# Kernel optimization log

Measured on AMD Instinct MI355X. Metric: run time of the kernel, lower is better.

Reference implementation:

```python
import jax, jax.numpy as jnp
import numpy as np

B, S, D, H, C = 2, 2048, 1024, 16, 64

def setup_inputs() -> dict:
    key = jax.random.key(0)
    kx, kq, kk, kv, ko = jax.random.split(key, 5)
    scale = 0.02
    return {
        "x": jax.random.normal(kx, (B, S, D), dtype=jnp.float32),
        "Wq": jax.random.normal(kq, (D, H, C), dtype=jnp.float32) * scale,
        "Wk": jax.random.normal(kk, (D, H, C), dtype=jnp.float32) * scale,
        "Wv": jax.random.normal(kv, (D, H, C), dtype=jnp.float32) * scale,
        "Wo": jax.random.normal(ko, (H, C, D), dtype=jnp.float32) * scale,
    }

def reference(x, Wq, Wk, Wv, Wo):
    # project to per-head q/k/v: [B,S,H,C]
    q = jnp.einsum('bqd,dhc->bqhc', x, Wq)
    k = jnp.einsum('bkd,dhc->bkhc', x, Wk)
    v = jnp.einsum('bkd,dhc->bkhc', x, Wv)
    q = q * (C ** -0.5)
    alphas = jnp.einsum('bqhc,bkhc->bhqk', q, k)  # [B,H,S,S]
    weights = jax.nn.softmax(alphas, axis=-1)
    out = jnp.einsum('bhqk,bkhc->bqhc', weights, v)
    return jnp.einsum('bqhc,hcd->bqd', out, Wo)
```

## Files before the change

kernel.cpp:

```cpp
#include <hip/hip_runtime.h>
#include <hip/hip_bf16.h>
#include <stdint.h>
#include <stddef.h>

typedef __bf16 bf16;
typedef __bf16 bf16x4 __attribute__((ext_vector_type(4)));
typedef __bf16 bf16x8 __attribute__((ext_vector_type(8)));
typedef float f32x4 __attribute__((ext_vector_type(4)));

#define DEV __device__ __forceinline__

DEV void async16(const bf16* g, bf16* l) {
    __builtin_amdgcn_global_load_lds(
        (const __attribute__((address_space(1))) void*)g,
        (__attribute__((address_space(3))) void*)l,
        16, 0, 0);
}

DEV uint32_t pktrunc(float lo, float hi) {
    return __builtin_amdgcn_perm(__builtin_bit_cast(uint32_t, hi),
                                 __builtin_bit_cast(uint32_t, lo), 0x07060302u);
}


__global__ void prep(const float* __restrict__ x,
                     const float* __restrict__ Wq, const float* __restrict__ Wk,
                     const float* __restrict__ Wv, const float* __restrict__ Wo,
                     bf16* __restrict__ xb, bf16* __restrict__ WqkvT,
                     bf16* __restrict__ WoT) {
    __shared__ float t[32][33];
    if (blockIdx.z == 4) {
        const int bid = blockIdx.y * 32 + blockIdx.x;
#pragma unroll
        for (int i = 0; i < 4; ++i) {
            const int idx = ((bid * 4 + i) * 256 + threadIdx.x) * 4;
            const float4 v = *(const float4*)(x + idx);
            bf16 o4[4] = {(bf16)v.x, (bf16)v.y, (bf16)v.z, (bf16)v.w};
            *(uint2*)(xb + idx) = *(const uint2*)o4;
        }
        return;
    }
    const float* src;
    bf16* dst;
    float scale = 1.0f;
    switch (blockIdx.z) {
        case 0: src = Wq; dst = WqkvT; scale = 0.125f * 1.4426950408889634f; break;
        case 1: src = Wk; dst = WqkvT + 1024 * 1024; break;
        case 2: src = Wv; dst = WqkvT + 2 * 1024 * 1024; break;
        default: src = Wo; dst = WoT; break;
    }
    const int c0 = blockIdx.x * 32, r0 = blockIdx.y * 32;
    const int tx = threadIdx.x & 31, ty = threadIdx.x >> 5;
#pragma unroll
    for (int i = 0; i < 32; i += 8)
        t[ty + i][tx] = src[(size_t)(r0 + ty + i) * 1024 + c0 + tx];
    __syncthreads();
#pragma unroll
    for (int i = 0; i < 32; i += 8)
        dst[(size_t)(c0 + ty + i) * 1024 + r0 + tx] = (bf16)(t[tx][ty + i] * scale);
}


template <bool OUT_F32>
__global__ __launch_bounds__(256, 3) void gemm_bt(
    const bf16* __restrict__ A, const bf16* __restrict__ BT, void* __restrict__ Cout,
    int M, int N, int K, bf16* __restrict__ VTout) {
    __shared__ __attribute__((aligned(16))) bf16 As[2 * 128 * 32];
    __shared__ __attribute__((aligned(16))) bf16 Bs[2 * 128 * 32];
    const int tid = threadIdx.x;
    const int wid = tid >> 6;
    const int lane = tid & 63;
    const int quad = lane >> 4;
    const int l16 = lane & 15;
    const int wm = wid >> 1, wn = wid & 1;

    const int orig = blockIdx.x;
    const int xcd = orig & 7, pos = orig >> 3;
    const int row = (xcd >> 1) * 8 + (pos & 7);
    const int col = (xcd & 1) * 12 + (pos >> 3);
    const int m0 = row * 128, n0 = col * 128;

    const int srow = wid * 32 + (lane >> 2);
    const int skcol = (lane & 3) * 8;
    const bf16* ag = A + (size_t)(m0 + srow) * K + skcol;
    const bf16* bg = BT + (size_t)(n0 + srow) * K + skcol;

    f32x4 acc[4][4];
#pragma unroll
    for (int i = 0; i < 4; ++i)
#pragma unroll
        for (int j = 0; j < 4; ++j) acc[i][j] = (f32x4){0.f, 0.f, 0.f, 0.f};

    for (int k0 = 0; k0 < K; k0 += 64) {
#pragma unroll
        for (int p = 0; p < 2; ++p) {
            async16(ag + k0 + p * 32, &As[p * 4096 + (wid * 32) * 32]);
            async16(ag + (size_t)16 * K + k0 + p * 32, &As[p * 4096 + (wid * 32 + 16) * 32]);
            async16(bg + k0 + p * 32, &Bs[p * 4096 + (wid * 32) * 32]);
            async16(bg + (size_t)16 * K + k0 + p * 32, &Bs[p * 4096 + (wid * 32 + 16) * 32]);
        }
        __syncthreads();

#pragma unroll
        for (int ks = 0; ks < 2; ++ks) {
            bf16x8 af[4], bfr[4];
#pragma unroll
            for (int mi = 0; mi < 4; ++mi)
                af[mi] = *(const bf16x8*)&As[ks * 4096 + (wm * 64 + mi * 16 + l16) * 32 + quad * 8];
#pragma unroll
            for (int ni = 0; ni < 4; ++ni)
                bfr[ni] = *(const bf16x8*)&Bs[ks * 4096 + (wn * 64 + ni * 16 + l16) * 32 + quad * 8];
#pragma unroll
            for (int mi = 0; mi < 4; ++mi)
#pragma unroll
                for (int ni = 0; ni < 4; ++ni)
                    acc[mi][ni] = __builtin_amdgcn_mfma_f32_16x16x32_bf16(
                        af[mi], bfr[ni], acc[mi][ni], 0, 0, 0);
        }
        __syncthreads();
    }

    if (VTout && n0 >= 2048) {
#pragma unroll
        for (int mi = 0; mi < 4; ++mi)
#pragma unroll
            for (int ni = 0; ni < 4; ++ni) {
                bf16 pk[4] = {(bf16)acc[mi][ni][0], (bf16)acc[mi][ni][1],
                              (bf16)acc[mi][ni][2], (bf16)acc[mi][ni][3]};
                *(uint2*)&VTout[(size_t)(n0 - 2048 + wn * 64 + ni * 16 + l16) * 4096 +
                                (m0 + wm * 64 + mi * 16 + quad * 4)] = *(const uint2*)pk;
            }
        return;
    }
    if (OUT_F32) {
        float* C = (float*)Cout;
#pragma unroll
        for (int mi = 0; mi < 4; ++mi)
#pragma unroll
            for (int ni = 0; ni < 4; ++ni)
#pragma unroll
                for (int r = 0; r < 4; ++r)
                    C[(size_t)(m0 + wm * 64 + mi * 16 + quad * 4 + r) * N +
                      (n0 + wn * 64 + ni * 16 + l16)] = acc[mi][ni][r];
    } else {
        bf16* C = (bf16*)Cout;
#pragma unroll
        for (int mi = 0; mi < 4; ++mi)
#pragma unroll
            for (int ni = 0; ni < 4; ++ni)
#pragma unroll
                for (int r = 0; r < 4; ++r)
                    C[(size_t)(m0 + wm * 64 + mi * 16 + quad * 4 + r) * N +
                      (n0 + wn * 64 + ni * 16 + l16)] = (bf16)acc[mi][ni][r];
    }
}


__global__ __launch_bounds__(256, 4) void gemm_tm2(
    const bf16* __restrict__ A, const bf16* __restrict__ BT, float* __restrict__ C,
    int M, int N, int K) {
    __shared__ __attribute__((aligned(16))) bf16 As[2 * 64 * 32];
    __shared__ __attribute__((aligned(16))) bf16 Bs[2 * 128 * 32];
    const int tid = threadIdx.x;
    const int wid = tid >> 6;
    const int lane = tid & 63;
    const int quad = lane >> 4;
    const int l16 = lane & 15;
    const int wm = wid >> 1, wn = wid & 1;

    const int orig = blockIdx.x;
    const int xcd = orig & 7, pos = orig >> 3;
    const int row = (xcd >> 1) * 16 + (pos & 15);
    const int col = (xcd & 1) * 4 + (pos >> 4);
    const int m0 = row * 64, n0 = col * 128;

    const int srowA = wid * 16 + (lane >> 2);
    const int srowB = wid * 32 + (lane >> 2);
    const int skcol = (lane & 3) * 8;
    const bf16* ag = A + (size_t)(m0 + srowA) * K + skcol;
    const bf16* bg = BT + (size_t)(n0 + srowB) * K + skcol;

    f32x4 acc[2][4];
#pragma unroll
    for (int i = 0; i < 2; ++i)
#pragma unroll
        for (int j = 0; j < 4; ++j) acc[i][j] = (f32x4){0.f, 0.f, 0.f, 0.f};

    for (int k0 = 0; k0 < K; k0 += 64) {
#pragma unroll
        for (int p = 0; p < 2; ++p) {
            async16(ag + k0 + p * 32, &As[p * 2048 + (wid * 16) * 32]);
            async16(bg + k0 + p * 32, &Bs[p * 4096 + (wid * 32) * 32]);
            async16(bg + (size_t)16 * K + k0 + p * 32, &Bs[p * 4096 + (wid * 32 + 16) * 32]);
        }
        __syncthreads();

#pragma unroll
        for (int ks = 0; ks < 2; ++ks) {
            bf16x8 af[2], bfr[4];
#pragma unroll
            for (int mi = 0; mi < 2; ++mi)
                af[mi] = *(const bf16x8*)&As[ks * 2048 + (wm * 32 + mi * 16 + l16) * 32 + quad * 8];
#pragma unroll
            for (int ni = 0; ni < 4; ++ni)
                bfr[ni] = *(const bf16x8*)&Bs[ks * 4096 + (wn * 64 + ni * 16 + l16) * 32 + quad * 8];
#pragma unroll
            for (int mi = 0; mi < 2; ++mi)
#pragma unroll
                for (int ni = 0; ni < 4; ++ni)
                    acc[mi][ni] = __builtin_amdgcn_mfma_f32_16x16x32_bf16(
                        af[mi], bfr[ni], acc[mi][ni], 0, 0, 0);
        }
        __syncthreads();
    }

#pragma unroll
    for (int mi = 0; mi < 2; ++mi)
#pragma unroll
        for (int ni = 0; ni < 4; ++ni)
#pragma unroll
            for (int r = 0; r < 4; ++r)
                C[(size_t)(m0 + wm * 32 + mi * 16 + quad * 4 + r) * N +
                  (n0 + wn * 64 + ni * 16 + l16)] = acc[mi][ni][r];
}


__global__ __launch_bounds__(256, 2) void flash_attn(
    const bf16* __restrict__ QKV, const bf16* __restrict__ VT, bf16* __restrict__ att) {
    constexpr int LDK = 72;
    constexpr int LDV = 136;
    __shared__ __attribute__((aligned(16))) char smem[36864];
    bf16* Ks = (bf16*)smem;
    bf16* Vs = (bf16*)(smem + 18432);
    float* Osc = (float*)smem;
    float* Lred = (float*)(smem + 32768);

    const int tid = threadIdx.x, wid = tid >> 6, lane = tid & 63;
    const int quad = lane >> 4, l16 = lane & 15;
    const int qh = wid >> 1, kh = wid & 1;
    const int bh = blockIdx.x, qt = blockIdx.y;
    const int b = bh >> 4, h = bh & 15;
    const int q0 = qt * 128;

    bf16x8 qf[4][2];
    {
        const bf16* qbase = QKV + (size_t)(b * 2048 + q0 + qh * 64 + l16) * 3072 + h * 64 + quad * 8;
#pragma unroll
        for (int mi = 0; mi < 4; ++mi)
#pragma unroll
            for (int ks = 0; ks < 2; ++ks)
                qf[mi][ks] = *(const bf16x8*)(qbase + (size_t)mi * 16 * 3072 + ks * 32);
    }

    const int krow = tid >> 3, kcol = (tid & 7) * 8;
    const int vrow = tid >> 4, vcol = (tid & 15) * 8;
    const bf16* kg = QKV + (size_t)(b * 2048 + krow) * 3072 + 1024 + h * 64 + kcol;
    const bf16* vg = VT + (size_t)(h * 64 + vrow) * 4096 + b * 2048 + vcol;

    bf16x8 kr[4], vr[4];
#pragma unroll
    for (int p = 0; p < 4; ++p) {
        kr[p] = *(const bf16x8*)(kg + (size_t)(32 * p) * 3072);
        vr[p] = *(const bf16x8*)(vg + (size_t)(16 * p) * 4096);
    }

    const bf16 one = (bf16)1.0f;
    const bf16x8 onesf = (bf16x8){one, one, one, one, one, one, one, one};

    f32x4 o[4][4];
    f32x4 ls[4];
#pragma unroll
    for (int mi = 0; mi < 4; ++mi) {
        ls[mi] = (f32x4){0.f, 0.f, 0.f, 0.f};
#pragma unroll
        for (int ct = 0; ct < 4; ++ct) o[mi][ct] = (f32x4){0.f, 0.f, 0.f, 0.f};
    }

    for (int it = 0; it < 16; ++it) {
#pragma unroll
        for (int p = 0; p < 4; ++p) {
            *(bf16x8*)&Ks[(32 * p + krow) * LDK + kcol] = kr[p];
            *(bf16x8*)&Vs[(16 * p + vrow) * LDV + vcol] = vr[p];
        }
        __syncthreads();

        if (it < 15) {
            const size_t ko = (size_t)(it + 1) * 128;
#pragma unroll
            for (int p = 0; p < 4; ++p) {
                kr[p] = *(const bf16x8*)(kg + (ko + 32 * p) * 3072);
                vr[p] = *(const bf16x8*)(vg + (size_t)(16 * p) * 4096 + ko);
            }
        }

#pragma unroll
        for (int pr = 0; pr < 2; ++pr) {
            const int kb = kh * 64 + pr * 32;
            const bf16x8 kfA0 = *(const bf16x8*)&Ks[(kb + l16) * LDK + quad * 8];
            const bf16x8 kfA1 = *(const bf16x8*)&Ks[(kb + l16) * LDK + 32 + quad * 8];
            const bf16x8 kfB0 = *(const bf16x8*)&Ks[(kb + 16 + l16) * LDK + quad * 8];
            const bf16x8 kfB1 = *(const bf16x8*)&Ks[(kb + 16 + l16) * LDK + 32 + quad * 8];
            bf16x8 vf[4];
#pragma unroll
            for (int ct = 0; ct < 4; ++ct) {
                const bf16x4 lo = *(const bf16x4*)&Vs[(ct * 16 + l16) * LDV + kb + quad * 4];
                const bf16x4 hi = *(const bf16x4*)&Vs[(ct * 16 + l16) * LDV + kb + 16 + quad * 4];
                vf[ct] = (bf16x8){lo[0], lo[1], lo[2], lo[3], hi[0], hi[1], hi[2], hi[3]};
            }
            __builtin_amdgcn_s_setprio(1);
#pragma unroll
            for (int mi = 0; mi < 4; ++mi) {
                f32x4 sA = (f32x4){0.f, 0.f, 0.f, 0.f};
                f32x4 sB = (f32x4){0.f, 0.f, 0.f, 0.f};
                sA = __builtin_amdgcn_mfma_f32_16x16x32_bf16(kfA0, qf[mi][0], sA, 0, 0, 0);
                sA = __builtin_amdgcn_mfma_f32_16x16x32_bf16(kfA1, qf[mi][1], sA, 0, 0, 0);
                sB = __builtin_amdgcn_mfma_f32_16x16x32_bf16(kfB0, qf[mi][0], sB, 0, 0, 0);
                sB = __builtin_amdgcn_mfma_f32_16x16x32_bf16(kfB1, qf[mi][1], sB, 0, 0, 0);

                const float pa0 = __builtin_amdgcn_exp2f(sA[0]);
                const float pa1 = __builtin_amdgcn_exp2f(sA[1]);
                const float pa2 = __builtin_amdgcn_exp2f(sA[2]);
                const float pa3 = __builtin_amdgcn_exp2f(sA[3]);
                const float pb0 = __builtin_amdgcn_exp2f(sB[0]);
                const float pb1 = __builtin_amdgcn_exp2f(sB[1]);
                const float pb2 = __builtin_amdgcn_exp2f(sB[2]);
                const float pb3 = __builtin_amdgcn_exp2f(sB[3]);

                union { uint32_t u[4]; bf16x8 v; } pu;
                pu.u[0] = pktrunc(pa0, pa1);
                pu.u[1] = pktrunc(pa2, pa3);
                pu.u[2] = pktrunc(pb0, pb1);
                pu.u[3] = pktrunc(pb2, pb3);
                const bf16x8 pf = pu.v;
#pragma unroll
                for (int ct = 0; ct < 4; ++ct)
                    o[mi][ct] = __builtin_amdgcn_mfma_f32_16x16x32_bf16(pf, vf[ct], o[mi][ct], 0, 0, 0);
                ls[mi] = __builtin_amdgcn_mfma_f32_16x16x32_bf16(pf, onesf, ls[mi], 0, 0, 0);
            }
            __builtin_amdgcn_s_setprio(0);
        }
        __syncthreads();
    }

    if (l16 == 0) {
#pragma unroll
        for (int mi = 0; mi < 4; ++mi)
#pragma unroll
            for (int r = 0; r < 4; ++r)
                Lred[wid * 64 + mi * 16 + quad * 4 + r] = ls[mi][r];
    }
    if (kh == 1) {
        float* dst = Osc + qh * 4096;
#pragma unroll
        for (int mi = 0; mi < 4; ++mi)
#pragma unroll
            for (int ct = 0; ct < 4; ++ct)
                *(f32x4*)(dst + (mi * 4 + ct) * 256 + lane * 4) = o[mi][ct];
    }
    __syncthreads();

    if (kh == 0) {
        const float* src = Osc + qh * 4096;
#pragma unroll
        for (int mi = 0; mi < 4; ++mi)
#pragma unroll
            for (int ct = 0; ct < 4; ++ct)
                o[mi][ct] += *(const f32x4*)(src + (mi * 4 + ct) * 256 + lane * 4);
#pragma unroll
        for (int mi = 0; mi < 4; ++mi)
#pragma unroll
            for (int r = 0; r < 4; ++r) {
                const int qrow = mi * 16 + quad * 4 + r;
                const float l = Lred[(qh * 2) * 64 + qrow] + Lred[(qh * 2 + 1) * 64 + qrow];
                const float inv = 1.0f / l;
                bf16* orow = att + (size_t)(b * 2048 + q0 + qh * 64 + qrow) * 1024 + h * 64 + l16;
#pragma unroll
                for (int ct = 0; ct < 4; ++ct)
                    orow[ct * 16] = (bf16)(o[mi][ct][r] * inv);
            }
    }
}


extern "C" void kernel_launch(void* const* d_in, const int* in_sizes, int n_in,
                              void* d_out, int out_size, void* d_ws, size_t ws_size,
                              hipStream_t stream) {
    (void)in_sizes; (void)n_in; (void)out_size; (void)ws_size;
    const float* x  = (const float*)d_in[0];
    const float* Wq = (const float*)d_in[1];
    const float* Wk = (const float*)d_in[2];
    const float* Wv = (const float*)d_in[3];
    const float* Wo = (const float*)d_in[4];

    char* ws = (char*)d_ws;
    bf16* xb    = (bf16*)(ws);
    bf16* att   = xb;
    bf16* WqkvT = (bf16*)(ws + (size_t)8  * 1024 * 1024);
    bf16* WoT   = (bf16*)(ws + (size_t)14 * 1024 * 1024);
    bf16* QKV   = (bf16*)(ws + (size_t)16 * 1024 * 1024);
    bf16* VT    = (bf16*)(ws + (size_t)40 * 1024 * 1024);

    prep<<<dim3(32, 32, 5), 256, 0, stream>>>(x, Wq, Wk, Wv, Wo, xb, WqkvT, WoT);

    gemm_bt<false><<<768, 256, 0, stream>>>(
        xb, WqkvT, QKV, 4096, 3072, 1024, VT);

    flash_attn<<<dim3(32, 16), 256, 0, stream>>>(QKV, VT, att);

    gemm_tm2<<<512, 256, 0, stream>>>(
        att, WoT, (float*)d_out, 4096, 1024, 1024);
}
```

Baseline: 175.6 us.

## Replace QKV projection GEMM with 256x256-tile, 8-wave, 4-stage pipelined kernel

The QKV projection GEMM moves from 128x128 tiles with 4 waves and a simple load-then-compute loop to 256x256 tiles with 8 waves per block. It uses a 4-buffer LDS ring (128 KB) that prefetches two k-steps ahead, with XOR-swizzled LDS addressing to avoid bank conflicts. Loads and MFMA groups are interleaved with barriers and s_setprio. The aim is to raise data reuse per tile and hide global-load latency, at the cost of only 192 blocks (fewer than the CU count) and heavy LDS and register use per block.

```diff
diff --git a/kernel.cpp b/kernel.cpp
--- a/kernel.cpp
+++ b/kernel.cpp
@@ -61,98 +61,115 @@
 }
 
 
-template <bool OUT_F32>
-__global__ __launch_bounds__(256, 3) void gemm_bt(
-    const bf16* __restrict__ A, const bf16* __restrict__ BT, void* __restrict__ Cout,
-    int M, int N, int K, bf16* __restrict__ VTout) {
-    __shared__ __attribute__((aligned(16))) bf16 As[2 * 128 * 32];
-    __shared__ __attribute__((aligned(16))) bf16 Bs[2 * 128 * 32];
+__global__ __launch_bounds__(512, 2) void gemm_bt8(
+    const bf16* __restrict__ A, const bf16* __restrict__ BT, bf16* __restrict__ C,
+    bf16* __restrict__ VTout) {
+    __shared__ __attribute__((aligned(16))) char smem[131072];
     const int tid = threadIdx.x;
-    const int wid = tid >> 6;
-    const int lane = tid & 63;
-    const int quad = lane >> 4;
-    const int l16 = lane & 15;
-    const int wm = wid >> 1, wn = wid & 1;
-
-    const int orig = blockIdx.x;
-    const int xcd = orig & 7, pos = orig >> 3;
-    const int row = (xcd >> 1) * 8 + (pos & 7);
-    const int col = (xcd & 1) * 12 + (pos >> 3);
-    const int m0 = row * 128, n0 = col * 128;
-
-    const int srow = wid * 32 + (lane >> 2);
-    const int skcol = (lane & 3) * 8;
-    const bf16* ag = A + (size_t)(m0 + srow) * K + skcol;
-    const bf16* bg = BT + (size_t)(n0 + srow) * K + skcol;
-
-    f32x4 acc[4][4];
-#pragma unroll
-    for (int i = 0; i < 4; ++i)
+    const int wid = tid >> 6, lane = tid & 63;
+    const int quad = lane >> 4, l16 = lane & 15;
+    const int wm = wid >> 2, wn = wid & 3;
+    const int m0 = (blockIdx.x & 15) * 256;
+    const int n0 = (blockIdx.x >> 4) * 256;
+
+    const int srow = tid >> 2;
+    const int chsw = (tid & 3) ^ ((srow >> 1) & 3);
+    const bf16* agA1 = A + (size_t)(m0 + srow) * 1024 + chsw * 8;
+    const bf16* agA2 = A + (size_t)(m0 + 128 + srow) * 1024 + chsw * 8;
+    const bf16* bgB1 = BT + (size_t)(n0 + srow) * 1024 + chsw * 8;
+    const bf16* bgB2 = BT + (size_t)(n0 + 128 + srow) * 1024 + chsw * 8;
+
+    const int chq = quad ^ ((l16 >> 1) & 3);
+    const int rbA = (wm * 128 + l16) * 32 + chq * 8;
+    const int rbB = (wn * 64 + l16) * 32 + chq * 8;
+
+    f32x4 acc[8][4];
+#pragma unroll
+    for (int i = 0; i < 8; ++i)
 #pragma unroll
         for (int j = 0; j < 4; ++j) acc[i][j] = (f32x4){0.f, 0.f, 0.f, 0.f};
 
-    for (int k0 = 0; k0 < K; k0 += 64) {
-#pragma unroll
-        for (int p = 0; p < 2; ++p) {
-            async16(ag + k0 + p * 32, &As[p * 4096 + (wid * 32) * 32]);
-            async16(ag + (size_t)16 * K + k0 + p * 32, &As[p * 4096 + (wid * 32 + 16) * 32]);
-            async16(bg + k0 + p * 32, &Bs[p * 4096 + (wid * 32) * 32]);
-            async16(bg + (size_t)16 * K + k0 + p * 32, &Bs[p * 4096 + (wid * 32 + 16) * 32]);
-        }
-        __syncthreads();
-
-#pragma unroll
-        for (int ks = 0; ks < 2; ++ks) {
-            bf16x8 af[4], bfr[4];
-#pragma unroll
-            for (int mi = 0; mi < 4; ++mi)
-                af[mi] = *(const bf16x8*)&As[ks * 4096 + (wm * 64 + mi * 16 + l16) * 32 + quad * 8];
+#define STAGE_A8(ts, bufp) do { \
+    async16(agA1 + (size_t)(ts) * 32, (bf16*)(bufp) + wid * 512); \
+    async16(agA2 + (size_t)(ts) * 32, (bf16*)(bufp) + 4096 + wid * 512); } while (0)
+#define STAGE_B8(ts, bufp) do { \
+    async16(bgB1 + (size_t)(ts) * 32, (bf16*)(bufp) + wid * 512); \
+    async16(bgB2 + (size_t)(ts) * 32, (bf16*)(bufp) + 4096 + wid * 512); } while (0)
+
+    STAGE_A8(0, smem);
+    STAGE_B8(0, smem + 16384);
+    STAGE_A8(1, smem + 32768);
+    STAGE_B8(1, smem + 32768 + 16384);
+    asm volatile("s_waitcnt vmcnt(4)" ::: "memory");
+    __builtin_amdgcn_s_barrier();
+
+    for (int t = 0; t < 32; ++t) {
+        const char* bufc = smem + (size_t)(t & 3) * 32768;
+        char* bufp = smem + (size_t)((t + 2) & 3) * 32768;
+        const bf16* Ab = (const bf16*)bufc;
+        const bf16* Bb = (const bf16*)(bufc + 16384);
+        const int tsrc = (t + 2) & 31;
+
+        bf16x8 bfr[4], afr[4];
+#pragma unroll
+        for (int ni = 0; ni < 4; ++ni)
+            bfr[ni] = *(const bf16x8*)(Bb + rbB + ni * 512);
+#pragma unroll
+        for (int mi = 0; mi < 4; ++mi)
+            afr[mi] = *(const bf16x8*)(Ab + rbA + mi * 512);
+        STAGE_A8(tsrc, bufp);
+        __builtin_amdgcn_s_barrier();
+        __builtin_amdgcn_s_setprio(1);
+#pragma unroll
+        for (int mi = 0; mi < 4; ++mi)
 #pragma unroll
             for (int ni = 0; ni < 4; ++ni)
-                bfr[ni] = *(const bf16x8*)&Bs[ks * 4096 + (wn * 64 + ni * 16 + l16) * 32 + quad * 8];
-#pragma unroll
-            for (int mi = 0; mi < 4; ++mi)
-#pragma unroll
-                for (int ni = 0; ni < 4; ++ni)
-                    acc[mi][ni] = __builtin_amdgcn_mfma_f32_16x16x32_bf16(
-                        af[mi], bfr[ni], acc[mi][ni], 0, 0, 0);
-        }
-        __syncthreads();
-    }
-
-    if (VTout && n0 >= 2048) {
-#pragma unroll
-        for (int mi = 0; mi < 4; ++mi)
+                acc[mi][ni] = __builtin_amdgcn_mfma_f32_16x16x32_bf16(
+                    afr[mi], bfr[ni], acc[mi][ni], 0, 0, 0);
+        __builtin_amdgcn_s_setprio(0);
+        __builtin_amdgcn_s_barrier();
+
+        bf16x8 afr2[4];
+#pragma unroll
+        for (int mi = 0; mi < 4; ++mi)
+            afr2[mi] = *(const bf16x8*)(Ab + rbA + (mi + 4) * 512);
+        STAGE_B8(tsrc, bufp + 16384);
+        __builtin_amdgcn_s_barrier();
+        __builtin_amdgcn_s_setprio(1);
+#pragma unroll
+        for (int mi = 0; mi < 4; ++mi)
+#pragma unroll
+            for (int ni = 0; ni < 4; ++ni)
+                acc[mi + 4][ni] = __builtin_amdgcn_mfma_f32_16x16x32_bf16(
+                    afr2[mi], bfr[ni], acc[mi + 4][ni], 0, 0, 0);
+        __builtin_amdgcn_s_setprio(0);
+        asm volatile("s_waitcnt vmcnt(4)" ::: "memory");
+        __builtin_amdgcn_s_barrier();
+        __builtin_amdgcn_sched_barrier(0);
+    }
+#undef STAGE_A8
+#undef STAGE_B8
+
+    if (n0 >= 2048) {
+#pragma unroll
+        for (int mi = 0; mi < 8; ++mi)
 #pragma unroll
             for (int ni = 0; ni < 4; ++ni) {
                 bf16 pk[4] = {(bf16)acc[mi][ni][0], (bf16)acc[mi][ni][1],
                               (bf16)acc[mi][ni][2], (bf16)acc[mi][ni][3]};
                 *(uint2*)&VTout[(size_t)(n0 - 2048 + wn * 64 + ni * 16 + l16) * 4096 +
-                                (m0 + wm * 64 + mi * 16 + quad * 4)] = *(const uint2*)pk;
+                                (m0 + wm * 128 + mi * 16 + quad * 4)] = *(const uint2*)pk;
             }
         return;
     }
-    if (OUT_F32) {
-        float* C = (float*)Cout;
-#pragma unroll
-        for (int mi = 0; mi < 4; ++mi)
-#pragma unroll
-            for (int ni = 0; ni < 4; ++ni)
-#pragma unroll
-                for (int r = 0; r < 4; ++r)
-                    C[(size_t)(m0 + wm * 64 + mi * 16 + quad * 4 + r) * N +
-                      (n0 + wn * 64 + ni * 16 + l16)] = acc[mi][ni][r];
-    } else {
-        bf16* C = (bf16*)Cout;
-#pragma unroll
-        for (int mi = 0; mi < 4; ++mi)
-#pragma unroll
-            for (int ni = 0; ni < 4; ++ni)
-#pragma unroll
-                for (int r = 0; r < 4; ++r)
-                    C[(size_t)(m0 + wm * 64 + mi * 16 + quad * 4 + r) * N +
-                      (n0 + wn * 64 + ni * 16 + l16)] = (bf16)acc[mi][ni][r];
-    }
+#pragma unroll
+    for (int mi = 0; mi < 8; ++mi)
+#pragma unroll
+        for (int ni = 0; ni < 4; ++ni)
+#pragma unroll
+            for (int r = 0; r < 4; ++r)
+                C[(size_t)(m0 + wm * 128 + mi * 16 + quad * 4 + r) * 3072 +
+                  (n0 + wn * 64 + ni * 16 + l16)] = (bf16)acc[mi][ni][r];
 }
 
 
@@ -402,8 +419,7 @@
 
     prep<<<dim3(32, 32, 5), 256, 0, stream>>>(x, Wq, Wk, Wv, Wo, xb, WqkvT, WoT);
 
-    gemm_bt<false><<<768, 256, 0, stream>>>(
-        xb, WqkvT, QKV, 4096, 3072, 1024, VT);
+    gemm_bt8<<<16 * 12, 512, 0, stream>>>(xb, WqkvT, QKV, VT);
 
     flash_attn<<<dim3(32, 16), 256, 0, stream>>>(QKV, VT, att);
 
```

Measured after the change: 175.2 us. Within noise of the previous version (-0.2%).
